# Kernel tuning notes

Measured on AMD Instinct MI355X. Metric: run time of the kernel, lower is better.

The kernel has to match this reference:

```python
import jax, jax.numpy as jnp
import numpy as np

B, C, H, W = 8, 256, 64, 64
NH = 8            # num_heads
OC = 256          # out_channels
D = C // NH       # per-head channel dim = 32
HW = H * W
BN_EPS = 1e-5


def _conv1x1(x, Wt, b):
    # x: [B,Cin,H,W], Wt: [Cout,Cin]
    return jnp.einsum('bchw,oc->bohw', x, Wt) + b[None, :, None, None]


def setup_inputs() -> dict:
    key = jax.random.key(0)
    ks = jax.random.split(key, 16)
    def n(k, shape, s=0.05):
        return jax.random.normal(k, shape, dtype=jnp.float32) * s
    return {
        'F1': jax.random.normal(ks[0], (B, C, H, W), jnp.float32),
        'F2': jax.random.normal(ks[1], (B, C, H, W), jnp.float32),
        'Wq':  n(ks[2], (C, 2 * C)), 'bq':  n(ks[3], (C,)),
        'Wk1': n(ks[4], (C, C)),     'bk1': n(ks[5], (C,)),
        'Wv1': n(ks[6], (C, C)),     'bv1': n(ks[7], (C,)),
        'Wk2': n(ks[8], (C, C)),     'bk2': n(ks[9], (C,)),
        'Wv2': n(ks[10], (C, C)),    'bv2': n(ks[11], (C,)),
        'mu':  jnp.full((1,), 0.5, jnp.float32),   # learnable scalar (init 0 in torch; nonzero here for nontrivial math)
        'Wc':  n(ks[12], (OC, 2 * C, 3, 3)),
        'gamma': jnp.ones((OC,), jnp.float32),
        'beta':  jnp.zeros((OC,), jnp.float32),
        'rmean': jnp.zeros((OC,), jnp.float32),
        'rvar':  jnp.ones((OC,), jnp.float32),
    }


def reference(F1, F2, Wq, bq, Wk1, bk1, Wv1, bv1, Wk2, bk2, Wv2, bv2,
              mu, Wc, gamma, beta, rmean, rvar):
    # fused query from both streams
    Qf = _conv1x1(jnp.concatenate([F1, F2], axis=1), Wq, bq)          # [B,C,H,W]
    Q = Qf.reshape(B, NH, D, HW).transpose(0, 1, 3, 2)                # [B,h,HW,d]
    Qs = jax.nn.softmax(Q, axis=-1)                                   # softmax over d

    def branch(F, Wk, bk, Wv, bv):
        K = _conv1x1(F, Wk, bk).reshape(B, NH, D, HW)                 # [B,h,d,HW]
        V = _conv1x1(F, Wv, bv).reshape(B, NH, D, HW)                 # [B,h,d,HW]
        Ks = jax.nn.softmax(K, axis=-1)                               # softmax over HW
        Att = jnp.einsum('bhdn,bhne->bhde', Ks, Qs)                   # [B,h,d,d]
        Xw = jnp.einsum('bhde,bhen->bhdn', Att, V)                    # [B,h,d,HW]
        return Xw.reshape(B, C, H, W)

    X1 = branch(F1, Wk1, bk1, Wv1, bv1)
    X2 = branch(F2, Wk2, bk2, Wv2, bv2)

    fused = jnp.concatenate([mu * X1 + F1, mu * X2 + F2], axis=1)     # [B,2C,H,W]
    y = jax.lax.conv_general_dilated(
        fused, Wc, window_strides=(1, 1), padding='SAME',
        dimension_numbers=('NCHW', 'OIHW', 'NCHW'))                   # [B,OC,H,W]
    # inference-mode BatchNorm + ReLU
    inv = gamma / jnp.sqrt(rvar + BN_EPS)
    y = y * inv[None, :, None, None] + (beta - rmean * inv)[None, :, None, None]
    return jax.nn.relu(y)
```

## Files before the change

kernel.cpp:

```cpp
#include <hip/hip_runtime.h>

typedef __attribute__((ext_vector_type(8))) short bf8;
typedef __attribute__((ext_vector_type(4))) float f32x4;

static __device__ __forceinline__ unsigned short f2b(float x) {
    unsigned u = __builtin_bit_cast(unsigned, x);
    u += 0x7fffu + ((u >> 16) & 1u);
    return (unsigned short)(u >> 16);
}

static __device__ __forceinline__ void gload_lds16(const void* g, void* l) {
    __builtin_amdgcn_global_load_lds(
        (const __attribute__((address_space(1))) unsigned int*)g,
        (__attribute__((address_space(3))) unsigned int*)l, 16, 0, 0);
}

__global__ __launch_bounds__(256) void k_prep(
    const float* __restrict__ Wq, const float* __restrict__ Wk1, const float* __restrict__ Wv1,
    const float* __restrict__ Wk2, const float* __restrict__ Wv2, const float* __restrict__ Wc,
    const float* __restrict__ gamma, const float* __restrict__ beta,
    const float* __restrict__ rmean, const float* __restrict__ rvar,
    const float* __restrict__ F1, const float* __restrict__ F2,
    unsigned short* __restrict__ WQB, unsigned short* __restrict__ WKB, unsigned short* __restrict__ WVB,
    unsigned short* __restrict__ WCB, float* __restrict__ BNS, float* __restrict__ BNB,
    float* __restrict__ SUMK, unsigned short* __restrict__ XT)
{
    const int bid = blockIdx.x;
    if (bid < 4096) {
        __shared__ float tile[64][65];
        const int b = bid >> 9;
        const int c0 = ((bid >> 6) & 7) * 64;
        const int p0 = (bid & 63) * 64;
        const int tx = threadIdx.x & 63;
        const int ty = threadIdx.x >> 6;
        const float* src = (c0 < 256) ? F1 : F2;
        const int cb = c0 & 255;
#pragma unroll
        for (int i = 0; i < 16; i++) {
            int cl = i * 4 + ty;
            tile[cl][tx] = src[((size_t)b * 256 + cb + cl) * 4096 + p0 + tx];
        }
        __syncthreads();
        const int t = threadIdx.x;
        const int p = t >> 2;
        const int cg = (t & 3) * 16;
        unsigned short tmp[16];
#pragma unroll
        for (int j = 0; j < 16; j++) tmp[j] = f2b(tile[cg + j][p]);
        unsigned short* dst = XT + ((size_t)b * 4096 + p0 + p) * 512 + c0 + cg;
        *(uint4*)dst = *(const uint4*)tmp;
        *(uint4*)(dst + 8) = *(const uint4*)(tmp + 8);
        return;
    }
    const int total = 131072 + 4 * 65536 + 1179648 + 256 + 4096;
    for (int i = (bid - 4096) * 256 + threadIdx.x; i < total; i += 256 * 256) {
        int j = i;
        if (j < 131072) { WQB[j] = f2b(Wq[j]); continue; }
        j -= 131072;
        if (j < 65536) { WKB[j] = f2b(Wk1[j]); continue; }
        j -= 65536;
        if (j < 65536) { WKB[65536 + j] = f2b(Wk2[j]); continue; }
        j -= 65536;
        if (j < 65536) { WVB[j] = f2b(Wv1[j]); continue; }
        j -= 65536;
        if (j < 65536) { WVB[65536 + j] = f2b(Wv2[j]); continue; }
        j -= 65536;
        if (j < 1179648) {
            int cl = j & 63;
            int rest = j >> 6;
            int o = rest & 255;
            int tc = rest >> 8;
            int tap = tc >> 3, ccb = tc & 7;
            int c = ccb * 64 + cl;
            WCB[j] = f2b(Wc[(size_t)(o * 512 + c) * 9 + tap]);
            continue;
        }
        j -= 1179648;
        if (j < 256) {
            float inv = gamma[j] * rsqrtf(rvar[j] + 1e-5f);
            BNS[j] = inv;
            BNB[j] = beta[j] - rmean[j] * inv;
            continue;
        }
        j -= 256;
        SUMK[j] = 0.0f;
    }
}

template<int MODE>
__global__ __launch_bounds__(256) void k_gemm1x1(
    const unsigned short* __restrict__ A,
    const unsigned short* __restrict__ XT,
    const float* __restrict__ bias,
    const float* __restrict__ bias2,
    unsigned short* __restrict__ outU,
    float* __restrict__ outF,
    const unsigned short* __restrict__ QSp,
    float* __restrict__ ATTP,
    int Kd)
{
    __shared__ unsigned short lds[2][2][128 * 64];
    int br = 0, b = blockIdx.z, myy = blockIdx.y;
    if (MODE == 3) { br = blockIdx.z >> 3; b = blockIdx.z & 7; }
    if (MODE == 4) { br = blockIdx.y >> 1; myy = blockIdx.y & 1; }
    const int m0 = myy * 128;
    const int n0 = blockIdx.x * 128;
    const int co = (MODE == 2) ? 0 : br * 256;
    const unsigned short* Ab = A + (size_t)br * 65536;
    const float* bi = br ? bias2 : bias;
    const int lane = threadIdx.x & 63;
    const int wv = threadIdx.x >> 6;
    const int wr = wv >> 1, wc = wv & 1;
    const int lrow = lane & 15, kg = lane >> 4;
    const int px = lane >> 3, sl = lane & 7;
    const int nt = Kd >> 6;

    f32x4 acc[4][4];
#pragma unroll
    for (int mi = 0; mi < 4; mi++)
#pragma unroll
        for (int ni = 0; ni < 4; ni++)
            acc[mi][ni] = (f32x4){0.f, 0.f, 0.f, 0.f};

#pragma unroll
    for (int j = 0; j < 4; j++) {
        int r0 = wv * 32 + j * 8;
        gload_lds16(Ab + (size_t)(m0 + r0 + px) * Kd + (sl ^ px) * 8, &lds[0][0][r0 * 64]);
        gload_lds16(XT + ((size_t)b * 4096 + n0 + r0 + px) * 512 + co + (sl ^ px) * 8, &lds[0][1][r0 * 64]);
    }
    __syncthreads();

    int cb = 0;
    for (int kt = 0; kt < nt; kt++) {
        if (kt + 1 < nt) {
            int k0 = (kt + 1) << 6;
            int nb = cb ^ 1;
#pragma unroll
            for (int j = 0; j < 4; j++) {
                int r0 = wv * 32 + j * 8;
                gload_lds16(Ab + (size_t)(m0 + r0 + px) * Kd + k0 + (sl ^ px) * 8, &lds[nb][0][r0 * 64]);
                gload_lds16(XT + ((size_t)b * 4096 + n0 + r0 + px) * 512 + co + k0 + (sl ^ px) * 8, &lds[nb][1][r0 * 64]);
            }
        }
        const unsigned short* wa = lds[cb][0];
        const unsigned short* wb = lds[cb][1];
#pragma unroll
        for (int klo = 0; klo < 64; klo += 32) {
            const int slin = klo >> 3;
            bf8 a[4], bv[4];
#pragma unroll
            for (int mi = 0; mi < 4; mi++) {
                int ol = wr * 64 + mi * 16 + lrow;
                a[mi] = *(const bf8*)(wa + ol * 64 + (((slin + kg) ^ (ol & 7)) * 8));
            }
#pragma unroll
            for (int ni = 0; ni < 4; ni++) {
                int nl = wc * 64 + ni * 16 + lrow;
                bv[ni] = *(const bf8*)(wb + nl * 64 + (((slin + kg) ^ (nl & 7)) * 8));
            }
#pragma unroll
            for (int mi = 0; mi < 4; mi++)
#pragma unroll
                for (int ni = 0; ni < 4; ni++)
                    acc[mi][ni] = __builtin_amdgcn_mfma_f32_16x16x32_bf16(a[mi], bv[ni], acc[mi][ni], 0, 0, 0);
        }
        __syncthreads();
        cb ^= 1;
    }

    if (MODE == 2) {
#pragma unroll
        for (int hh = 0; hh < 2; hh++) {
            float vv[2][4][4];
            float mx[4];
#pragma unroll
            for (int ni = 0; ni < 4; ni++) mx[ni] = -1e30f;
#pragma unroll
            for (int ms = 0; ms < 2; ms++) {
                int mi = hh * 2 + ms;
                int row0 = m0 + wr * 64 + mi * 16 + kg * 4;
#pragma unroll
                for (int r = 0; r < 4; r++) {
                    float bb = bi[row0 + r];
#pragma unroll
                    for (int ni = 0; ni < 4; ni++) {
                        float x = acc[mi][ni][r] + bb;
                        vv[ms][r][ni] = x;
                        mx[ni] = fmaxf(mx[ni], x);
                    }
                }
            }
#pragma unroll
            for (int ni = 0; ni < 4; ni++) {
                mx[ni] = fmaxf(mx[ni], __shfl_xor(mx[ni], 16, 64));
                mx[ni] = fmaxf(mx[ni], __shfl_xor(mx[ni], 32, 64));
            }
            float sm[4] = {0.f, 0.f, 0.f, 0.f};
#pragma unroll
            for (int ms = 0; ms < 2; ms++)
#pragma unroll
                for (int r = 0; r < 4; r++)
#pragma unroll
                    for (int ni = 0; ni < 4; ni++) {
                        float e = __expf(vv[ms][r][ni] - mx[ni]);
                        vv[ms][r][ni] = e;
                        sm[ni] += e;
                    }
#pragma unroll
            for (int ni = 0; ni < 4; ni++) {
                sm[ni] += __shfl_xor(sm[ni], 16, 64);
                sm[ni] += __shfl_xor(sm[ni], 32, 64);
                sm[ni] = 1.0f / sm[ni];
            }
            int h = (m0 + wr * 64 + hh * 32) >> 5;
#pragma unroll
            for (int ms = 0; ms < 2; ms++) {
                int e0 = ms * 16 + kg * 4;
#pragma unroll
                for (int r = 0; r < 4; r++)
#pragma unroll
                    for (int ni = 0; ni < 4; ni++) {
                        int col = n0 + wc * 64 + ni * 16 + lrow;
                        outU[((size_t)(b * 8 + h) * 32 + e0 + r) * 4096 + col] = f2b(vv[ms][r][ni] * sm[ni]);
                    }
            }
        }
    } else if (MODE == 3) {
        unsigned short* P = &lds[0][0][0];
        float* red = (float*)&lds[1][0][0];
        float ps[4][4];
#pragma unroll
        for (int mi = 0; mi < 4; mi++) {
            int rowl0 = wr * 64 + mi * 16 + kg * 4;
#pragma unroll
            for (int r = 0; r < 4; r++) {
                float bb = bi[m0 + rowl0 + r];
                int row = rowl0 + r;
                float s = 0.f;
#pragma unroll
                for (int ni = 0; ni < 4; ni++) {
                    float e = __expf(acc[mi][ni][r] + bb);
                    int col = wc * 64 + ni * 16 + lrow;
                    int slot = (col >> 3) ^ (row & 7);
                    P[row * 128 + slot * 8 + (col & 7)] = f2b(e);
                    s += e;
                }
                ps[mi][r] = s;
            }
        }
#pragma unroll
        for (int mi = 0; mi < 4; mi++)
#pragma unroll
            for (int r = 0; r < 4; r++)
                red[(wr * 64 + mi * 16 + kg * 4 + r) * 33 + wc * 16 + lrow] = ps[mi][r];
        __syncthreads();
        if (threadIdx.x < 128) {
            float s = 0.f;
#pragma unroll
            for (int j = 0; j < 32; j++) s += red[threadIdx.x * 33 + j];
            atomicAdd(&outF[br * 2048 + b * 256 + m0 + threadIdx.x], s);
        }
        const int hh = wv;
        const int bh = b * 8 + (m0 >> 5) + hh;
        const unsigned short* QSb = QSp + ((size_t)bh * 32) * 4096 + n0;
        f32x4 acc2[2][2];
#pragma unroll
        for (int mi2 = 0; mi2 < 2; mi2++)
#pragma unroll
            for (int ni2 = 0; ni2 < 2; ni2++)
                acc2[mi2][ni2] = (f32x4){0.f, 0.f, 0.f, 0.f};
#pragma unroll
        for (int ks = 0; ks < 4; ks++) {
            bf8 pa[2], qb[2];
#pragma unroll
            for (int mi2 = 0; mi2 < 2; mi2++) {
                int row = hh * 32 + mi2 * 16 + lrow;
                int slot = (ks * 4 + kg) ^ (row & 7);
                pa[mi2] = *(const bf8*)(P + row * 128 + slot * 8);
            }
#pragma unroll
            for (int ni2 = 0; ni2 < 2; ni2++)
                qb[ni2] = *(const bf8*)(QSb + (size_t)(ni2 * 16 + lrow) * 4096 + ks * 32 + kg * 8);
#pragma unroll
            for (int mi2 = 0; mi2 < 2; mi2++)
#pragma unroll
                for (int ni2 = 0; ni2 < 2; ni2++)
                    acc2[mi2][ni2] = __builtin_amdgcn_mfma_f32_16x16x32_bf16(pa[mi2], qb[ni2], acc2[mi2][ni2], 0, 0, 0);
        }
        float* dst = ATTP + (size_t)br * 2097152 + ((size_t)bh * 32 + (n0 >> 7)) * 1024;
#pragma unroll
        for (int mi2 = 0; mi2 < 2; mi2++)
#pragma unroll
            for (int ni2 = 0; ni2 < 2; ni2++)
#pragma unroll
                for (int r = 0; r < 4; r++)
                    dst[(mi2 * 16 + kg * 4 + r) * 32 + ni2 * 16 + lrow] = acc2[mi2][ni2][r];
    } else {
        unsigned short* vlds = &lds[0][0][0];
#pragma unroll
        for (int mi = 0; mi < 4; mi++) {
#pragma unroll
            for (int ni = 0; ni < 4; ni++) {
                int ch0 = wr * 64 + mi * 16 + kg * 4;
                int p = wc * 64 + ni * 16 + lrow;
                int sg = ch0 >> 3;
                unsigned long long pk = 0;
#pragma unroll
                for (int r = 0; r < 4; r++) {
                    unsigned short us = f2b(acc[mi][ni][r] + bi[m0 + ch0 + r]);
                    pk |= (unsigned long long)us << (16 * r);
                }
                *(unsigned long long*)(vlds + p * 128 + ((sg ^ (p & 15)) * 8) + (ch0 & 7)) = pk;
            }
        }
        __syncthreads();
        const int hl = wv;
        const int bh = b * 8 + (m0 >> 5) + hl;
        const unsigned short* ATTh = QSp + (size_t)br * 65536 + (size_t)bh * 1024;
        bf8 af[2];
#pragma unroll
        for (int mi2 = 0; mi2 < 2; mi2++)
            af[mi2] = *(const bf8*)(ATTh + (mi2 * 16 + lrow) * 32 + kg * 8);
#pragma unroll
        for (int ni2 = 0; ni2 < 8; ni2++) {
            int pp = ni2 * 16 + lrow;
            bf8 bf = *(const bf8*)(vlds + pp * 128 + (((hl * 4 + kg) ^ (pp & 15)) * 8));
            f32x4 pa0 = (f32x4){0.f, 0.f, 0.f, 0.f};
            f32x4 pa1 = (f32x4){0.f, 0.f, 0.f, 0.f};
            pa0 = __builtin_amdgcn_mfma_f32_16x16x32_bf16(af[0], bf, pa0, 0, 0, 0);
            pa1 = __builtin_amdgcn_mfma_f32_16x16x32_bf16(af[1], bf, pa1, 0, 0, 0);
#pragma unroll
            for (int mi2 = 0; mi2 < 2; mi2++) {
                f32x4 pa = mi2 ? pa1 : pa0;
                int c0 = co + m0 + hl * 32 + mi2 * 16 + kg * 4;
                size_t base = ((size_t)b * 4096 + n0 + pp) * 512 + c0;
                unsigned long long rin = *(const unsigned long long*)(XT + base);
                unsigned long long pk = 0;
#pragma unroll
                for (int r = 0; r < 4; r++) {
                    unsigned short us = (unsigned short)(rin >> (16 * r));
                    float f = __builtin_bit_cast(float, ((unsigned)us) << 16);
                    pk |= (unsigned long long)f2b(pa[r] + f) << (16 * r);
                }
                *(unsigned long long*)(outU + base) = pk;
            }
        }
    }
}

__global__ __launch_bounds__(256) void k_att_red(const float* __restrict__ ATTP,
                                                 const float* __restrict__ SUMK,
                                                 const float* __restrict__ mup,
                                                 unsigned short* __restrict__ ATT)
{
    const int gid = blockIdx.x;
    const int br = gid >> 6, bh = gid & 63;
    const int b = bh >> 3, h = bh & 7;
    const int tid = threadIdx.x;
    const float mu = mup[0];
    const float* src = ATTP + (size_t)br * 2097152;
#pragma unroll
    for (int i = 0; i < 4; i++) {
        int idx = tid + i * 256;
        int d = idx >> 5;
        float s = 0.f;
        for (int nch = 0; nch < 32; nch++)
            s += src[((size_t)bh * 32 + nch) * 1024 + idx];
        ATT[(size_t)br * 65536 + (size_t)bh * 1024 + idx] = f2b(mu * s / SUMK[br * 2048 + b * 256 + h * 32 + d]);
    }
}

__global__ __launch_bounds__(256) void k_conv3(
    const unsigned short* __restrict__ WB2,
    const unsigned short* __restrict__ FUSED,
    const float* __restrict__ BNS, const float* __restrict__ BNB,
    float* __restrict__ out)
{
    __shared__ unsigned short lds_in[4 * 72 * 64];
    __shared__ unsigned short lds_w[2][128 * 64];

    const int b = blockIdx.z;
    const int m0 = blockIdx.y * 128;
    const int ry = blockIdx.x;
    const int lane = threadIdx.x & 63;
    const int wv = threadIdx.x >> 6;
    const int wr = wv >> 1, wc = wv & 1;
    const int lrow = lane & 15, kg = lane >> 4;
    const int px = lane >> 3, sl = lane & 7;

    f32x4 acc[4][4];
#pragma unroll
    for (int mi = 0; mi < 4; mi++)
#pragma unroll
        for (int ni = 0; ni < 4; ni++)
            acc[mi][ni] = (f32x4){0.f, 0.f, 0.f, 0.f};

    for (int ccb = 0; ccb < 8; ccb++) {
        for (int u = wv; u < 36; u += 4) {
            int rl = u / 9, seg = u - rl * 9;
            int gy = ry * 2 + rl - 1;
            bool rowok = ((unsigned)gy < 64u);
            int xi0 = seg * 8;
            unsigned short* ldsb = lds_in + (rl * 72 + xi0) * 64;
            int x = xi0 + px - 4;
            const unsigned short* src = FUSED
                + ((size_t)(b * 4096 + gy * 64 + x)) * 512 + ccb * 64 + (sl ^ px) * 8;
            if (rowok && seg >= 1 && seg <= 7) {
                gload_lds16(src, ldsb);
            } else {
                uint4 v = {0u, 0u, 0u, 0u};
                if (rowok && ((unsigned)x < 64u)) v = *(const uint4*)src;
                *(uint4*)(ldsb + lane * 8) = v;
            }
        }
        {
            const unsigned short* base = WB2 + (((size_t)(0 * 8 + ccb) * 256) + m0) * 64;
#pragma unroll
            for (int j = 0; j < 4; j++) {
                int o0 = wv * 32 + j * 8;
                gload_lds16(base + (size_t)(o0 + px) * 64 + (sl ^ px) * 8, &lds_w[0][o0 * 64]);
            }
        }
        __syncthreads();

        for (int tap = 0; tap < 9; tap++) {
            if (tap < 8) {
                const unsigned short* base = WB2 + (((size_t)((tap + 1) * 8 + ccb) * 256) + m0) * 64;
                unsigned short* wdst = lds_w[(tap + 1) & 1];
#pragma unroll
                for (int j = 0; j < 4; j++) {
                    int o0 = wv * 32 + j * 8;
                    gload_lds16(base + (size_t)(o0 + px) * 64 + (sl ^ px) * 8, &wdst[o0 * 64]);
                }
            }
            const unsigned short* wb = lds_w[tap & 1];
            const int ky = tap / 3, kx = tap - ky * 3;
            const int rl = wc + ky;
#pragma unroll
            for (int k0 = 0; k0 < 64; k0 += 32) {
                const int slin = k0 >> 3;
                bf8 a[4], bv[4];
#pragma unroll
                for (int mi = 0; mi < 4; mi++) {
                    int ol = wr * 64 + mi * 16 + lrow;
                    int s = (slin + kg) ^ (ol & 7);
                    a[mi] = *(const bf8*)(wb + ol * 64 + s * 8);
                }
#pragma unroll
                for (int ni = 0; ni < 4; ni++) {
                    int xi = ni * 16 + lrow + kx + 3;
                    int s = (slin + kg) ^ (xi & 7);
                    bv[ni] = *(const bf8*)(lds_in + (rl * 72 + xi) * 64 + s * 8);
                }
#pragma unroll
                for (int mi = 0; mi < 4; mi++)
#pragma unroll
                    for (int ni = 0; ni < 4; ni++)
                        acc[mi][ni] = __builtin_amdgcn_mfma_f32_16x16x32_bf16(a[mi], bv[ni], acc[mi][ni], 0, 0, 0);
            }
            __syncthreads();
        }
    }

#pragma unroll
    for (int mi = 0; mi < 4; mi++) {
#pragma unroll
        for (int ni = 0; ni < 4; ni++) {
            int o0 = m0 + wr * 64 + mi * 16 + kg * 4;
            int p = (ry * 2 + wc) * 64 + ni * 16 + lrow;
#pragma unroll
            for (int r = 0; r < 4; r++) {
                int o = o0 + r;
                float v = acc[mi][ni][r] * BNS[o] + BNB[o];
                out[((size_t)b * 256 + o) * 4096 + p] = fmaxf(v, 0.0f);
            }
        }
    }
}

extern "C" void kernel_launch(void* const* d_in, const int* in_sizes, int n_in,
                              void* d_out, int out_size, void* d_ws, size_t ws_size,
                              hipStream_t stream)
{
    (void)in_sizes; (void)n_in; (void)out_size; (void)ws_size;
    const float* F1 = (const float*)d_in[0];
    const float* F2 = (const float*)d_in[1];
    const float* Wq = (const float*)d_in[2];
    const float* bq = (const float*)d_in[3];
    const float* Wk1 = (const float*)d_in[4];
    const float* bk1 = (const float*)d_in[5];
    const float* Wv1 = (const float*)d_in[6];
    const float* bv1 = (const float*)d_in[7];
    const float* Wk2 = (const float*)d_in[8];
    const float* bk2 = (const float*)d_in[9];
    const float* Wv2 = (const float*)d_in[10];
    const float* bv2 = (const float*)d_in[11];
    const float* mu = (const float*)d_in[12];
    const float* Wc = (const float*)d_in[13];
    const float* gamma = (const float*)d_in[14];
    const float* beta = (const float*)d_in[15];
    const float* rmean = (const float*)d_in[16];
    const float* rvar = (const float*)d_in[17];

    char* ws = (char*)d_ws;
    size_t off = 0;
    auto give = [&](size_t bytes) -> char* {
        char* p = ws + off;
        off = (off + bytes + 255) & ~(size_t)255;
        return p;
    };
    unsigned short* XT     = (unsigned short*)give(33554432);
    unsigned short* FUSED2 = (unsigned short*)give(33554432);
    unsigned short* QS  = (unsigned short*)give(16777216);
    unsigned short* WQB = (unsigned short*)give(262144);
    unsigned short* WKB = (unsigned short*)give(262144);
    unsigned short* WVB = (unsigned short*)give(262144);
    unsigned short* WCB = (unsigned short*)give(2359296);
    unsigned short* ATT = (unsigned short*)give(262144);
    float* BNS = (float*)give(1024);
    float* BNB = (float*)give(1024);
    float* ATTP = (float*)give(16777216);
    float* SUMK = (float*)give(16384);

    k_prep<<<4352, 256, 0, stream>>>(Wq, Wk1, Wv1, Wk2, Wv2, Wc, gamma, beta, rmean, rvar,
                                     F1, F2, WQB, WKB, WVB, WCB, BNS, BNB, SUMK, XT);
    k_gemm1x1<2><<<dim3(32, 2, 8), 256, 0, stream>>>(WQB, XT, bq, nullptr, QS, nullptr, nullptr, nullptr, 512);
    k_gemm1x1<3><<<dim3(32, 2, 16), 256, 0, stream>>>(WKB, XT, bk1, bk2, nullptr, SUMK, QS, ATTP, 256);
    k_att_red<<<128, 256, 0, stream>>>(ATTP, SUMK, mu, ATT);
    k_gemm1x1<4><<<dim3(32, 4, 8), 256, 0, stream>>>(WVB, XT, bv1, bv2, FUSED2, nullptr, ATT, nullptr, 256);
    k_conv3<<<dim3(32, 2, 8), 256, 0, stream>>>(WCB, FUSED2, BNS, BNB, (float*)d_out);
}
```

Measured before the change: 175.8 us.

## Use triple-buffered half-K weight ring with explicit vmcnt waits in conv3x3

The prep kernel now lays out conv weights in 32-channel half-blocks. The conv kernel streams those half-tap weight slices through a 3-slot LDS ring, prefetching two stages ahead and replacing __syncthreads with s_waitcnt vmcnt plus raw barriers. The goal is to hide weight-load latency behind MFMA work and cut synchronisation cost. The weight tile no longer uses the XOR swizzle, so LDS bank conflicts on A reads may rise. The hand-counted vmcnt waits are fragile because the halo staging also issues global loads.

Measured after the change: 184.3 us. 4.8% more time.

```diff
diff --git a/kernel.cpp b/kernel.cpp
--- a/kernel.cpp
+++ b/kernel.cpp
@@ -66,12 +66,12 @@
         if (j < 65536) { WVB[65536 + j] = f2b(Wv2[j]); continue; }
         j -= 65536;
         if (j < 1179648) {
-            int cl = j & 63;
-            int rest = j >> 6;
-            int o = rest & 255;
-            int tc = rest >> 8;
-            int tap = tc >> 3, ccb = tc & 7;
-            int c = ccb * 64 + cl;
+            int c5 = j & 31;
+            int o  = (j >> 5) & 255;
+            int kh = (j >> 13) & 1;
+            int tc = j >> 14;
+            int ccb = tc & 7, tap = tc >> 3;
+            int c = ccb * 64 + kh * 32 + c5;
             WCB[j] = f2b(Wc[(size_t)(o * 512 + c) * 9 + tap]);
             continue;
         }
@@ -377,7 +377,7 @@
     float* __restrict__ out)
 {
     __shared__ unsigned short lds_in[4 * 72 * 64];
-    __shared__ unsigned short lds_w[2][128 * 64];
+    __shared__ unsigned short wring[3][128 * 32];
 
     const int b = blockIdx.z;
     const int m0 = blockIdx.y * 128;
@@ -388,14 +388,17 @@
     const int lrow = lane & 15, kg = lane >> 4;
     const int px = lane >> 3, sl = lane & 7;
 
-    f32x4 acc[4][4];
-#pragma unroll
-    for (int mi = 0; mi < 4; mi++)
-#pragma unroll
-        for (int ni = 0; ni < 4; ni++)
-            acc[mi][ni] = (f32x4){0.f, 0.f, 0.f, 0.f};
-
-    for (int ccb = 0; ccb < 8; ccb++) {
+    auto stage_w2 = [&](int sg, int ccb) {
+        const unsigned short* base = WB2 +
+            ((((size_t)(sg >> 1) * 8 + ccb) * 2 + (sg & 1)) * 256 + m0) * 32;
+        unsigned short* dst = &wring[sg % 3][0];
+#pragma unroll
+        for (int it = 0; it < 2; it++) {
+            int off = (wv * 32 + it * 16) * 32;
+            gload_lds16(base + off + lane * 8, dst + off);
+        }
+    };
+    auto stage_halo = [&](int ccb) {
         for (int u = wv; u < 36; u += 4) {
             int rl = u / 9, seg = u - rl * 9;
             int gy = ry * 2 + rl - 1;
@@ -413,53 +416,52 @@
                 *(uint4*)(ldsb + lane * 8) = v;
             }
         }
-        {
-            const unsigned short* base = WB2 + (((size_t)(0 * 8 + ccb) * 256) + m0) * 64;
-#pragma unroll
-            for (int j = 0; j < 4; j++) {
-                int o0 = wv * 32 + j * 8;
-                gload_lds16(base + (size_t)(o0 + px) * 64 + (sl ^ px) * 8, &lds_w[0][o0 * 64]);
-            }
-        }
-        __syncthreads();
-
-        for (int tap = 0; tap < 9; tap++) {
-            if (tap < 8) {
-                const unsigned short* base = WB2 + (((size_t)((tap + 1) * 8 + ccb) * 256) + m0) * 64;
-                unsigned short* wdst = lds_w[(tap + 1) & 1];
-#pragma unroll
-                for (int j = 0; j < 4; j++) {
-                    int o0 = wv * 32 + j * 8;
-                    gload_lds16(base + (size_t)(o0 + px) * 64 + (sl ^ px) * 8, &wdst[o0 * 64]);
-                }
-            }
-            const unsigned short* wb = lds_w[tap & 1];
+    };
+
+    f32x4 acc[4][4];
+#pragma unroll
+    for (int mi = 0; mi < 4; mi++)
+#pragma unroll
+        for (int ni = 0; ni < 4; ni++)
+            acc[mi][ni] = (f32x4){0.f, 0.f, 0.f, 0.f};
+
+    for (int ccb = 0; ccb < 8; ccb++) {
+        stage_halo(ccb);
+        stage_w2(0, ccb);
+        stage_w2(1, ccb);
+        asm volatile("s_waitcnt vmcnt(0) lgkmcnt(0)" ::: "memory");
+        __builtin_amdgcn_s_barrier();
+
+#pragma unroll
+        for (int sg = 0; sg < 18; sg++) {
+            if (sg >= 1) {
+                if (sg <= 16) asm volatile("s_waitcnt vmcnt(2)" ::: "memory");
+                else          asm volatile("s_waitcnt vmcnt(0)" ::: "memory");
+                __builtin_amdgcn_s_barrier();
+            }
+            if (sg + 2 < 18) stage_w2(sg + 2, ccb);
+
+            const unsigned short* wb = &wring[sg % 3][0];
+            const int tap = sg >> 1, kh = sg & 1;
             const int ky = tap / 3, kx = tap - ky * 3;
             const int rl = wc + ky;
-#pragma unroll
-            for (int k0 = 0; k0 < 64; k0 += 32) {
-                const int slin = k0 >> 3;
-                bf8 a[4], bv[4];
-#pragma unroll
-                for (int mi = 0; mi < 4; mi++) {
-                    int ol = wr * 64 + mi * 16 + lrow;
-                    int s = (slin + kg) ^ (ol & 7);
-                    a[mi] = *(const bf8*)(wb + ol * 64 + s * 8);
-                }
-#pragma unroll
-                for (int ni = 0; ni < 4; ni++) {
-                    int xi = ni * 16 + lrow + kx + 3;
-                    int s = (slin + kg) ^ (xi & 7);
-                    bv[ni] = *(const bf8*)(lds_in + (rl * 72 + xi) * 64 + s * 8);
-                }
-#pragma unroll
-                for (int mi = 0; mi < 4; mi++)
-#pragma unroll
-                    for (int ni = 0; ni < 4; ni++)
-                        acc[mi][ni] = __builtin_amdgcn_mfma_f32_16x16x32_bf16(a[mi], bv[ni], acc[mi][ni], 0, 0, 0);
-            }
-            __syncthreads();
-        }
+            bf8 a[4], bv[4];
+#pragma unroll
+            for (int mi = 0; mi < 4; mi++)
+                a[mi] = *(const bf8*)(wb + (wr * 64 + mi * 16 + lrow) * 32 + kg * 8);
+#pragma unroll
+            for (int ni = 0; ni < 4; ni++) {
+                int xi = ni * 16 + lrow + kx + 3;
+                int s = (kh * 4 + kg) ^ (xi & 7);
+                bv[ni] = *(const bf8*)(lds_in + (rl * 72 + xi) * 64 + s * 8);
+            }
+#pragma unroll
+            for (int mi = 0; mi < 4; mi++)
+#pragma unroll
+                for (int ni = 0; ni < 4; ni++)
+                    acc[mi][ni] = __builtin_amdgcn_mfma_f32_16x16x32_bf16(a[mi], bv[ni], acc[mi][ni], 0, 0, 0);
+        }
+        __builtin_amdgcn_s_barrier();
     }
 
 #pragma unroll
```
